# Performance work log

Hardware: AMD Instinct MI355X
Metric: run time of the kernel (lower is better)

The kernel has to match this reference:

```python
import math
import jax, jax.numpy as jnp
import numpy as np

NHEAD = 8


def setup_inputs() -> dict:
    key = jax.random.key(0)
    ks = jax.random.split(key, 16)
    B, S, M, Ss, Ksn, D = 8, 512, 8, 16, 16, 512
    f32 = jnp.float32
    w_scale = 0.05
    return {
        "q_temporal": jax.random.normal(ks[0], (B, S, M, D), f32),
        "k_temporal": jax.random.normal(ks[1], (B, S, M, D), f32),
        "v_temporal": jax.random.normal(ks[2], (B, S, M, D), f32),
        "q_static": jax.random.normal(ks[3], (B, Ss, D), f32),
        "k_static": jax.random.normal(ks[4], (B, Ksn, D), f32),
        "v_static": jax.random.normal(ks[5], (B, Ksn, D), f32),
        "mask_temporal": jax.random.randint(ks[6], (B, S, M), 0, 2).astype(jnp.int32),
        "mask_static": jax.random.randint(ks[7], (B, Ksn), 0, 2).astype(jnp.int32),
        "Wq": jax.random.normal(ks[8], (D, D), f32) * w_scale,
        "bq": jax.random.normal(ks[9], (D,), f32) * w_scale,
        "Wk": jax.random.normal(ks[10], (D, D), f32) * w_scale,
        "bk": jax.random.normal(ks[11], (D,), f32) * w_scale,
        "Wv": jax.random.normal(ks[12], (D, D), f32) * w_scale,
        "bv": jax.random.normal(ks[13], (D,), f32) * w_scale,
        "Wo": jax.random.normal(ks[14], (D, D), f32) * w_scale,
        "bo": jax.random.normal(ks[15], (D,), f32) * w_scale,
    }


def reference(q_temporal, k_temporal, v_temporal, q_static, k_static, v_static,
              mask_temporal, mask_static, Wq, bq, Wk, bk, Wv, bv, Wo, bo):
    B, S, M, D = q_temporal.shape
    dh = D // NHEAD
    scale = 1.0 / math.sqrt(dh)
    SM = S * M

    def lin(x, W, b):
        return x @ W + b

    def h5(x):  # [B,S,M,D] -> [B,H,S,M,dh]
        b, s, m, d = x.shape
        return x.reshape(b, s, m, NHEAD, dh).transpose(0, 3, 1, 2, 4)

    def h4(x):  # [B,N,D] -> [B,H,N,dh]
        b, n, d = x.shape
        return x.reshape(b, n, NHEAD, dh).transpose(0, 2, 1, 3)

    # additive masks: 1 -> 0 (keep), 0 -> -inf
    m_t = jnp.where(mask_temporal == 1, 0.0, -jnp.inf)  # [B,S,M]
    m_s = jnp.where(mask_static == 1, 0.0, -jnp.inf)    # [B,Ks]

    # shared static-key/value heads: [B,H,Ks,dh]
    Ks_h = h4(lin(k_static, Wk, bk))
    Vs_h = h4(lin(v_static, Wv, bv))

    # ---- temporal side ----
    Qt = h5(lin(q_temporal, Wq, bq))   # [B,H,S,M,dh]
    Kt = h5(lin(k_temporal, Wk, bk))
    Vt = h5(lin(v_temporal, Wv, bv))
    qt_kt = jnp.einsum('bhsmd,bhsnd->bhsmn', Qt, Kt) * scale + m_t[:, None, :, None, :]   # [B,H,S,M,M]
    qt_ks = jnp.einsum('bhsmd,bhkd->bhsmk', Qt, Ks_h) * scale + m_s[:, None, None, None, :]  # [B,H,S,M,Ks]
    w_t = jax.nn.softmax(jnp.concatenate([qt_kt, qt_ks], axis=-1), axis=-1)  # [B,H,S,M,M+Ks]
    qkv_t = (jnp.einsum('bhsmn,bhsnd->bhsmd', w_t[..., :M], Vt)
             + jnp.einsum('bhsmk,bhkd->bhsmd', w_t[..., M:], Vs_h))          # [B,H,S,M,dh]
    out_t = lin(qkv_t.transpose(0, 2, 3, 1, 4).reshape(B, S, M, D), Wo, bo)  # [B,S,M,D]

    # ---- static side ----
    Qs = h4(lin(q_static, Wq, bq))                              # [B,H,Ss,dh]
    Kt_f = h4(lin(k_temporal.reshape(B, SM, D), Wk, bk))        # [B,H,S*M,dh]
    Vt_f = h4(lin(v_temporal.reshape(B, SM, D), Wv, bv))
    qs_kt = jnp.einsum('bhqd,bhnd->bhqn', Qs, Kt_f) * scale + m_t.reshape(B, 1, 1, SM)  # [B,H,Ss,S*M]
    qs_ks = jnp.einsum('bhqd,bhkd->bhqk', Qs, Ks_h) * scale + m_s[:, None, None, :]     # [B,H,Ss,Ks]
    w_s = jax.nn.softmax(jnp.concatenate([qs_kt, qs_ks], axis=-1), axis=-1)  # [B,H,Ss,S*M+Ks]
    qkv_s = (jnp.einsum('bhqn,bhnd->bhqd', w_s[..., :SM], Vt_f)
             + jnp.einsum('bhqk,bhkd->bhqd', w_s[..., SM:], Vs_h))           # [B,H,Ss,dh]
    Ss = qkv_s.shape[2]
    out_s = lin(qkv_s.transpose(0, 2, 1, 3).reshape(B, Ss, D), Wo, bo)       # [B,Ss,D]

    return (out_t, w_t, out_s, w_s)
```

## Files before the change

### kernel.cpp

```cpp
#include <hip/hip_runtime.h>
#include <hip/hip_bf16.h>

typedef __attribute__((ext_vector_type(8))) __bf16 bf16x8;
typedef __attribute__((ext_vector_type(4))) float f32x4;

__device__ __forceinline__ float b2f(unsigned short u) {
    unsigned int x = ((unsigned int)u) << 16;
    float f;
    __builtin_memcpy(&f, &x, 4);
    return f;
}
__device__ __forceinline__ unsigned short f2b(float f) {
    __hip_bfloat16 h = __float2bfloat16(f);
    unsigned short u;
    __builtin_memcpy(&u, &h, 2);
    return u;
}
union U4 { uint4 v; unsigned short u[8]; };

__global__ __launch_bounds__(256) void transpose512cvt4(
    const float* __restrict__ i0, const float* __restrict__ i1,
    const float* __restrict__ i2, const float* __restrict__ i3,
    unsigned short* __restrict__ o0, unsigned short* __restrict__ o1,
    unsigned short* __restrict__ o2, unsigned short* __restrict__ o3)
{
    const float* in = i0;
    unsigned short* out = o0;
    if (blockIdx.z == 1) { in = i1; out = o1; }
    else if (blockIdx.z == 2) { in = i2; out = o2; }
    else if (blockIdx.z == 3) { in = i3; out = o3; }
    __shared__ float tile[32][33];
    int tx = threadIdx.x & 31, ty = threadIdx.x >> 5;
    int bx = blockIdx.x, by = blockIdx.y;
    #pragma unroll
    for (int i = 0; i < 32; i += 8)
        tile[ty + i][tx] = in[(size_t)(bx * 32 + ty + i) * 512 + by * 32 + tx];
    __syncthreads();
    #pragma unroll
    for (int i = 0; i < 32; i += 8)
        out[(size_t)(by * 32 + ty + i) * 512 + bx * 32 + tx] = f2b(tile[tx][ty + i]);
}


struct GemmSet {
    const void* A;
    const unsigned short* B;
    const float* bias;
    void* C;
    int cmode;
};

template<bool AF32>
__global__ __launch_bounds__(512, 2) void gemm_bp(
    GemmSet s0, GemmSet s1, GemmSet s2, int M, int mgroups)
{
    const int K = 512, N = 512;
    __shared__ __align__(16) unsigned short Bs[128 * 256];

    int NB = gridDim.x, bid = blockIdx.x;
    int wid;
    if ((NB & 31) == 0) {
        int x = bid & 7, tt = bid >> 3, r = tt & 3, j = tt >> 2;
        wid = (j * 8 + x) * 4 + r;
    } else wid = bid;
    int q = wid >> 2, np = wid & 3;
    int g = q / mgroups, mg = q - g * mgroups;
    GemmSet S = (g == 0) ? s0 : ((g == 1) ? s1 : s2);
    int n0 = np * 128, m0 = mg * 512;

    int t = threadIdx.x;
    int w = t >> 6, lane = t & 63, quad = lane >> 4, l16 = lane & 15;
    bool active = (m0 + w * 64) < M;
    size_t mrow = (size_t)(m0 + w * 64 + l16);

    const float* Ap32 = (const float*)S.A + mrow * K + quad * 8;
    const unsigned short* Ap16 = (const unsigned short*)S.A + mrow * K + quad * 8;

    int srow = t >> 2, sseg = t & 3;
    const unsigned short* Bg = S.B + (size_t)(n0 + srow) * K + sseg * 64;
    char* Bsb = (char*)Bs;
    unsigned int wbase = ((unsigned int)srow << 9) + ((unsigned int)sseg << 7);
    unsigned int wxor = ((unsigned int)(srow & 7)) << 4;
    unsigned int rxor = ((unsigned int)(l16 & 7)) << 4;

    f32x4 acc[4][8];
    #pragma unroll
    for (int i = 0; i < 4; ++i)
        #pragma unroll
        for (int j = 0; j < 8; ++j) acc[i][j] = (f32x4){0.f, 0.f, 0.f, 0.f};

    float4 pf[8];
    uint4 ph[4];

    auto ALOAD = [&](int kk) {
        if constexpr (AF32) {
            #pragma unroll
            for (int i = 0; i < 4; ++i) {
                const float4* pp = (const float4*)(Ap32 + (size_t)i * 16 * K + kk);
                pf[2 * i] = pp[0]; pf[2 * i + 1] = pp[1];
            }
        } else {
            #pragma unroll
            for (int i = 0; i < 4; ++i)
                ph[i] = *(const uint4*)(Ap16 + (size_t)i * 16 * K + kk);
        }
    };
    auto ACVT = [&](bf16x8* af) {
        if constexpr (AF32) {
            #pragma unroll
            for (int i = 0; i < 4; ++i) {
                U4 u;
                u.u[0] = f2b(pf[2*i].x);   u.u[1] = f2b(pf[2*i].y);
                u.u[2] = f2b(pf[2*i].z);   u.u[3] = f2b(pf[2*i].w);
                u.u[4] = f2b(pf[2*i+1].x); u.u[5] = f2b(pf[2*i+1].y);
                u.u[6] = f2b(pf[2*i+1].z); u.u[7] = f2b(pf[2*i+1].w);
                af[i] = *(bf16x8*)&u;
            }
        } else {
            #pragma unroll
            for (int i = 0; i < 4; ++i) af[i] = *(bf16x8*)&ph[i];
        }
    };
    auto STAGE = [&](int p) {
        uint4 v[8];
        #pragma unroll
        for (int i = 0; i < 8; ++i)
            v[i] = *(const uint4*)(Bg + p * 256 + i * 8);
        #pragma unroll
        for (int i = 0; i < 8; ++i)
            *(uint4*)(Bsb + ((wbase + i * 16) ^ wxor)) = v[i];
    };

    if (active) ALOAD(0);
    #pragma unroll
    for (int p = 0; p < 2; ++p) {
        __syncthreads();
        STAGE(p);
        __syncthreads();
        if (active) {
            int kb = p * 256;
            for (int ks = 0; ks < 8; ++ks) {
                bf16x8 af[4];
                ACVT(af);
                if (ks < 7) ALOAD(kb + (ks + 1) * 32);
                else if (p == 0) ALOAD(256);
                unsigned int kl2b = (unsigned int)((ks * 32 + quad * 8) * 2);
                #pragma unroll
                for (int j = 0; j < 8; ++j) {
                    unsigned int rb = (((unsigned int)(j * 16 + l16)) << 9) + kl2b;
                    bf16x8 bf = *(const bf16x8*)(Bsb + (rb ^ rxor));
                    #pragma unroll
                    for (int i = 0; i < 4; ++i)
                        acc[i][j] = __builtin_amdgcn_mfma_f32_16x16x32_bf16(af[i], bf, acc[i][j], 0, 0, 0);
                }
            }
        }
    }

    if (!active) return;
    int cmode = S.cmode;
    #pragma unroll
    for (int j = 0; j < 8; ++j) {
        int col = n0 + j * 16 + l16;
        float bc = S.bias[col];
        #pragma unroll
        for (int i = 0; i < 4; ++i) {
            int row = m0 + w * 64 + i * 16 + quad * 4;
            #pragma unroll
            for (int ii = 0; ii < 4; ++ii) {
                float v = acc[i][j][ii] + bc;
                int R = row + ii;
                if (cmode == 0) {
                    ((float*)S.C)[(size_t)R * N + col] = v;
                } else if (cmode == 1) {
                    ((unsigned short*)S.C)[(size_t)R * N + col] = f2b(v);
                } else {
                    int bb = R >> 12, n = R & 4095, hh = col >> 6, d = col & 63;
                    ((unsigned short*)S.C)[(((size_t)bb * 8 + hh) * 4096 + n) * 64 + d] = f2b(v);
                }
            }
        }
    }
}

__global__ __launch_bounds__(512) void temporal_attn(
    const unsigned short* __restrict__ Qt, const unsigned short* __restrict__ KH,
    const unsigned short* __restrict__ VH, const unsigned short* __restrict__ Ksp,
    const unsigned short* __restrict__ Vsp,
    const int* __restrict__ mask_t, const int* __restrict__ mask_s,
    float* __restrict__ w_t_out, unsigned short* __restrict__ qkv_t)
{
    int blk = blockIdx.x;
    int b = blk >> 8, sp = blk & 255;
    int s0 = sp * 2;
    int t = threadIdx.x;
    int h = t >> 6, lane = t & 63, quad = lane >> 4, l16 = lane & 15;

    __shared__ __align__(16) unsigned short Vt[8][64 * 40];
    __shared__ __align__(16) unsigned short Pl[8][16 * 40];

    size_t bh = (size_t)(b * 8 + h);
    size_t tok0 = ((size_t)(b * 512 + s0)) * 8;

    {
        int r = lane & 31, dh = (lane >> 5) * 32;
        const unsigned short* src = (r < 16)
            ? VH + (bh * 4096 + (size_t)(s0 * 8 + r)) * 64 + dh
            : Vsp + ((size_t)(b * 16 + (r - 16))) * 512 + h * 64 + dh;
        U4 u[4];
        #pragma unroll
        for (int g = 0; g < 4; ++g) u[g].v = ((const uint4*)src)[g];
        unsigned short* dst = &Vt[h][0];
        #pragma unroll
        for (int g = 0; g < 4; ++g)
            #pragma unroll
            for (int ii = 0; ii < 8; ++ii)
                dst[(dh + g * 8 + ii) * 40 + r] = u[g].u[ii];
    }

    const unsigned short* qp = Qt + (tok0 + l16) * 512 + h * 64 + quad * 8;
    bf16x8 qf0 = *(const bf16x8*)qp;
    bf16x8 qf1 = *(const bf16x8*)(qp + 32);
    const unsigned short* kpt = KH + (bh * 4096 + (size_t)(s0 * 8 + l16)) * 64 + quad * 8;
    bf16x8 kt0 = *(const bf16x8*)kpt;
    bf16x8 kt1 = *(const bf16x8*)(kpt + 32);
    const unsigned short* kps = Ksp + ((size_t)(b * 16 + l16)) * 512 + h * 64 + quad * 8;
    bf16x8 ks0 = *(const bf16x8*)kps;
    bf16x8 ks1 = *(const bf16x8*)(kps + 32);

    f32x4 sc0 = (f32x4){0.f, 0.f, 0.f, 0.f};
    f32x4 sc1 = (f32x4){0.f, 0.f, 0.f, 0.f};
    sc0 = __builtin_amdgcn_mfma_f32_16x16x32_bf16(qf0, kt0, sc0, 0, 0, 0);
    sc0 = __builtin_amdgcn_mfma_f32_16x16x32_bf16(qf1, kt1, sc0, 0, 0, 0);
    sc1 = __builtin_amdgcn_mfma_f32_16x16x32_bf16(qf0, ks0, sc1, 0, 0, 0);
    sc1 = __builtin_amdgcn_mfma_f32_16x16x32_bf16(qf1, ks1, sc1, 0, 0, 0);

    float madd0 = mask_t[tok0 + l16] ? 0.f : -1e30f;
    bool v0 = ((quad < 2) == (l16 < 8));
    if (!v0) madd0 = -1e30f;
    float madd1 = mask_s[b * 16 + l16] ? 0.f : -1e30f;

    float w0[4], w1[4];
    #pragma unroll
    for (int i = 0; i < 4; ++i) {
        float a = sc0[i] * 0.125f + madd0;
        float c = sc1[i] * 0.125f + madd1;
        float mx = fmaxf(a, c);
        mx = fmaxf(mx, __shfl_xor(mx, 1));
        mx = fmaxf(mx, __shfl_xor(mx, 2));
        mx = fmaxf(mx, __shfl_xor(mx, 4));
        mx = fmaxf(mx, __shfl_xor(mx, 8));
        float e0 = __expf(a - mx), e1 = __expf(c - mx);
        float se = e0 + e1;
        se += __shfl_xor(se, 1);
        se += __shfl_xor(se, 2);
        se += __shfl_xor(se, 4);
        se += __shfl_xor(se, 8);
        float inv = 1.f / se;
        w0[i] = e0 * inv;
        w1[i] = e1 * inv;
    }

    int row0 = quad * 4;
    #pragma unroll
    for (int i = 0; i < 4; ++i) {
        int row = row0 + i;
        Pl[h][row * 40 + l16] = f2b(w0[i]);
        Pl[h][row * 40 + 16 + l16] = f2b(w1[i]);
        int s = s0 + (row >> 3), m = row & 7;
        size_t wb = ((((size_t)b * 8 + h) * 512 + s) * 8 + m) * 24;
        if (v0) w_t_out[wb + (l16 & 7)] = w0[i];
        w_t_out[wb + 8 + l16] = w1[i];
    }

    bf16x8 pa = *(const bf16x8*)&Pl[h][l16 * 40 + quad * 8];
    f32x4 oacc[4];
    #pragma unroll
    for (int j = 0; j < 4; ++j) {
        bf16x8 vb = *(const bf16x8*)&Vt[h][(j * 16 + l16) * 40 + quad * 8];
        oacc[j] = (f32x4){0.f, 0.f, 0.f, 0.f};
        oacc[j] = __builtin_amdgcn_mfma_f32_16x16x32_bf16(pa, vb, oacc[j], 0, 0, 0);
    }
    #pragma unroll
    for (int j = 0; j < 4; ++j)
        #pragma unroll
        for (int ii = 0; ii < 4; ++ii) {
            int row = quad * 4 + ii;
            qkv_t[(tok0 + row) * 512 + h * 64 + j * 16 + l16] = f2b(oacc[j][ii]);
        }
}

__global__ __launch_bounds__(256) void static_attn_s1(
    const unsigned short* __restrict__ Qsp, const unsigned short* __restrict__ KH,
    const unsigned short* __restrict__ VH, const unsigned short* __restrict__ Ksp,
    const unsigned short* __restrict__ Vsp,
    const int* __restrict__ mask_t, const int* __restrict__ mask_s,
    float* __restrict__ w_s, float* __restrict__ Ppart, float* __restrict__ Lpart)
{
    int blk = blockIdx.x;
    int bh = blk & 63, c = blk >> 6;
    int b = bh >> 3, h = bh & 7;
    __shared__ __align__(16) unsigned short Klds[32 * 72];
    __shared__ __align__(16) unsigned short Vlds[64 * 40];
    __shared__ __align__(16) unsigned short Plds[16 * 40];
    __shared__ float maskv[32];
    __shared__ float sL[2][16];
    int t = threadIdx.x, wave = t >> 6, lane = t & 63, quad = lane >> 4, l16 = lane & 15;

    bf16x8 qf0 = *(const bf16x8*)(Qsp + ((size_t)(b * 16 + l16)) * 512 + h * 64 + quad * 8);
    bf16x8 qf1 = *(const bf16x8*)(Qsp + ((size_t)(b * 16 + l16)) * 512 + h * 64 + 32 + quad * 8);

    f32x4 pacc = (f32x4){0.f, 0.f, 0.f, 0.f};
    float Lacc[4] = {0.f, 0.f, 0.f, 0.f};
    int d0 = wave * 16;
    int sub = wave >> 1;
    int sr = t >> 3, spart = t & 7;
    int s0 = c * 16, s1 = (c == 7) ? 129 : (s0 + 16);

    for (int st = s0; st < s1; ++st) {
        int key0 = st * 32;
        int kk = key0 + sr;
        uint4 kv = {0, 0, 0, 0}, vv = {0, 0, 0, 0};
        if (kk < 4096) {
            kv = *(const uint4*)(KH + (((size_t)bh) * 4096 + kk) * 64 + spart * 8);
            vv = *(const uint4*)(VH + (((size_t)bh) * 4096 + kk) * 64 + spart * 8);
        } else if (kk < 4112) {
            kv = *(const uint4*)(Ksp + ((size_t)(b * 16 + kk - 4096)) * 512 + h * 64 + spart * 8);
            vv = *(const uint4*)(Vsp + ((size_t)(b * 16 + kk - 4096)) * 512 + h * 64 + spart * 8);
        }
        __syncthreads();
        *(uint4*)&Klds[sr * 72 + spart * 8] = kv;
        {
            U4 u; u.v = vv;
            #pragma unroll
            for (int ii = 0; ii < 8; ++ii) Vlds[(spart * 8 + ii) * 40 + sr] = u.u[ii];
        }
        if (t < 32) {
            int k2 = key0 + t;
            float ma = -1e30f;
            if (k2 < 4096) ma = mask_t[b * 4096 + k2] ? 0.f : -1e30f;
            else if (k2 < 4112) ma = mask_s[b * 16 + k2 - 4096] ? 0.f : -1e30f;
            maskv[t] = ma;
        }
        __syncthreads();
        if ((wave & 1) == 0) {
            bf16x8 kf0 = *(const bf16x8*)&Klds[(sub * 16 + l16) * 72 + quad * 8];
            bf16x8 kf1 = *(const bf16x8*)&Klds[(sub * 16 + l16) * 72 + 32 + quad * 8];
            f32x4 sc = (f32x4){0.f, 0.f, 0.f, 0.f};
            sc = __builtin_amdgcn_mfma_f32_16x16x32_bf16(qf0, kf0, sc, 0, 0, 0);
            sc = __builtin_amdgcn_mfma_f32_16x16x32_bf16(qf1, kf1, sc, 0, 0, 0);
            float ma = maskv[sub * 16 + l16];
            size_t wbase = (((size_t)bh) * 16 + quad * 4) * 4112 + key0 + sub * 16 + l16;
            #pragma unroll
            for (int i = 0; i < 4; ++i) {
                float sv = sc[i] * 0.125f + ma;
                float w = __expf(sv);
                Lacc[i] += w;
                w_s[wbase + (size_t)i * 4112] = w;
                Plds[(quad * 4 + i) * 40 + sub * 16 + l16] = f2b(w);
            }
        }
        __syncthreads();
        bf16x8 pf = *(const bf16x8*)&Plds[l16 * 40 + quad * 8];
        bf16x8 vf = *(const bf16x8*)&Vlds[(d0 + l16) * 40 + quad * 8];
        pacc = __builtin_amdgcn_mfma_f32_16x16x32_bf16(pf, vf, pacc, 0, 0, 0);
    }

    if ((wave & 1) == 0) {
        #pragma unroll
        for (int i = 0; i < 4; ++i) {
            float v = Lacc[i];
            v += __shfl_xor(v, 1);
            v += __shfl_xor(v, 2);
            v += __shfl_xor(v, 4);
            v += __shfl_xor(v, 8);
            Lacc[i] = v;
        }
        if (l16 == 0) {
            #pragma unroll
            for (int i = 0; i < 4; ++i) sL[wave >> 1][quad * 4 + i] = Lacc[i];
        }
    }
    size_t pbase = ((size_t)(bh * 8 + c) * 16 + quad * 4) * 64 + d0 + l16;
    #pragma unroll
    for (int i = 0; i < 4; ++i) Ppart[pbase + (size_t)i * 64] = pacc[i];
    __syncthreads();
    if (t < 16) Lpart[(bh * 8 + c) * 16 + t] = sL[0][t] + sL[1][t];
}

__global__ __launch_bounds__(256) void static_attn_s4(
    const float* __restrict__ Ppart, const float* __restrict__ Lpart,
    float* __restrict__ w_s, unsigned short* __restrict__ qkvS)
{
    int bh = blockIdx.x, b = bh >> 3, h = bh & 7;
    __shared__ float invL[16];
    int t = threadIdx.x;
    if (t < 16) {
        float L = 0.f;
        #pragma unroll
        for (int cc = 0; cc < 8; ++cc) L += Lpart[(bh * 8 + cc) * 16 + t];
        invL[t] = 1.f / L;
    }
    __syncthreads();
    #pragma unroll
    for (int i = 0; i < 4; ++i) {
        int idx = t + i * 256;
        int q = idx >> 6, d = idx & 63;
        float s = 0.f;
        #pragma unroll
        for (int cc = 0; cc < 8; ++cc) s += Ppart[((size_t)(bh * 8 + cc) * 16 + q) * 64 + d];
        qkvS[((size_t)(b * 16 + q)) * 512 + h * 64 + d] = f2b(s * invL[q]);
    }
    size_t base = (size_t)bh * 16 * 4112;
    for (int q = 0; q < 16; ++q) {
        float il = invL[q];
        for (int kk = t; kk < 4112; kk += 256) w_s[base + q * 4112 + kk] *= il;
    }
}

extern "C" void kernel_launch(void* const* d_in, const int* in_sizes, int n_in,
                              void* d_out, int out_size, void* d_ws, size_t ws_size,
                              hipStream_t stream)
{
    const float* q_t = (const float*)d_in[0];
    const float* k_t = (const float*)d_in[1];
    const float* v_t = (const float*)d_in[2];
    const float* q_s = (const float*)d_in[3];
    const float* k_s = (const float*)d_in[4];
    const float* v_s = (const float*)d_in[5];
    const int* m_t = (const int*)d_in[6];
    const int* m_s = (const int*)d_in[7];
    const float* Wq = (const float*)d_in[8];
    const float* bq = (const float*)d_in[9];
    const float* Wk = (const float*)d_in[10];
    const float* bk = (const float*)d_in[11];
    const float* Wv = (const float*)d_in[12];
    const float* bv = (const float*)d_in[13];
    const float* Wo = (const float*)d_in[14];
    const float* bo = (const float*)d_in[15];

    char* ws = (char*)d_ws;
    size_t off = 0;
    auto alloc = [&](size_t bytes) {
        void* p = ws + off;
        off += (bytes + 255) & ~(size_t)255;
        return p;
    };
    const size_t WB = (size_t)512 * 512 * 2;
    const size_t TB = (size_t)32768 * 512 * 2;
    const size_t SB = (size_t)128 * 512 * 2;
    unsigned short* WqT = (unsigned short*)alloc(WB);
    unsigned short* WkT = (unsigned short*)alloc(WB);
    unsigned short* WvT = (unsigned short*)alloc(WB);
    unsigned short* WoT = (unsigned short*)alloc(WB);
    unsigned short* Qt   = (unsigned short*)alloc(TB);
    unsigned short* KH   = (unsigned short*)alloc(TB);
    unsigned short* VH   = (unsigned short*)alloc(TB);
    unsigned short* qkvT = (unsigned short*)alloc(TB);
    unsigned short* Qsp  = (unsigned short*)alloc(SB);
    unsigned short* Ksp  = (unsigned short*)alloc(SB);
    unsigned short* Vsp  = (unsigned short*)alloc(SB);
    unsigned short* qkvS = (unsigned short*)alloc(SB);
    float* Ppart = (float*)alloc((size_t)64 * 8 * 16 * 64 * 4);
    float* Lpart = (float*)alloc((size_t)64 * 8 * 16 * 4);

    float* out    = (float*)d_out;
    float* out_tp = out;
    float* w_t_o  = out + 16777216;
    float* out_sp = out + 23068672;
    float* w_s_o  = out + 23134208;

    transpose512cvt4<<<dim3(16, 16, 4), 256, 0, stream>>>(Wq, Wk, Wv, Wo, WqT, WkT, WvT, WoT);

    GemmSet gq  = { q_t,  WqT, bq, Qt,   1 };
    GemmSet gk  = { k_t,  WkT, bk, KH,   2 };
    GemmSet gv  = { v_t,  WvT, bv, VH,   2 };
    GemmSet gqs = { q_s,  WqT, bq, Qsp,  1 };
    GemmSet gks = { k_s,  WkT, bk, Ksp,  1 };
    GemmSet gvs = { v_s,  WvT, bv, Vsp,  1 };
    GemmSet got = { qkvT, WoT, bo, out_tp, 0 };
    GemmSet gos = { qkvS, WoT, bo, out_sp, 0 };

    gemm_bp<true><<<dim3(768), 512, 0, stream>>>(gq, gk, gv, 32768, 64);
    gemm_bp<true><<<dim3(12), 512, 0, stream>>>(gqs, gks, gvs, 128, 1);

    temporal_attn<<<2048, 512, 0, stream>>>(Qt, KH, VH, Ksp, Vsp, m_t, m_s, w_t_o, qkvT);
    static_attn_s1<<<512, 256, 0, stream>>>(Qsp, KH, VH, Ksp, Vsp, m_t, m_s, w_s_o, Ppart, Lpart);
    static_attn_s4<<<64, 256, 0, stream>>>(Ppart, Lpart, w_s_o, qkvS);

    gemm_bp<false><<<dim3(256), 512, 0, stream>>>(got, got, got, 32768, 64);
    gemm_bp<false><<<dim3(4), 512, 0, stream>>>(gos, gos, gos, 128, 1);
}
```

Measured before the change: 582.7 us.

## Rewrite projection GEMMs with 128x128 tiles and async global-to-LDS double buffering

Replaces the 512-row by 128-column GEMM, which staged only B in LDS and kept A in registers, with a 128x128 tile kernel. Both A and B now stream through LDS in double-buffered 32-wide K slices using global_load_lds DMA with XOR swizzling. Block IDs are remapped so consecutive tiles land on the same XCD. The change is meant to cut register pressure, raise occupancy (256 threads, 3 blocks per CU), and overlap loads with MFMA work, at the cost of more blocks, more re-reads of A and B across tiles, and a barrier per K step.

```diff
diff --git a/kernel.cpp b/kernel.cpp
--- a/kernel.cpp
+++ b/kernel.cpp
@@ -17,6 +17,12 @@
     return u;
 }
 union U4 { uint4 v; unsigned short u[8]; };
+
+__device__ __forceinline__ void gload16(const void* g, void* l) {
+    __builtin_amdgcn_global_load_lds(
+        (const __attribute__((address_space(1))) unsigned int*)g,
+        (__attribute__((address_space(3))) unsigned int*)l, 16, 0, 0);
+}
 
 __global__ __launch_bounds__(256) void transpose512cvt4(
     const float* __restrict__ i0, const float* __restrict__ i1,
@@ -51,121 +57,116 @@
 };
 
 template<bool AF32>
-__global__ __launch_bounds__(512, 2) void gemm_bp(
-    GemmSet s0, GemmSet s1, GemmSet s2, int M, int mgroups)
+__global__ __launch_bounds__(256, 3) void gemm_lds(
+    GemmSet s0, GemmSet s1, GemmSet s2, int M)
 {
     const int K = 512, N = 512;
-    __shared__ __align__(16) unsigned short Bs[128 * 256];
+    __shared__ __align__(16) unsigned char AsB[AF32 ? 32768 : 16384];
+    __shared__ __align__(16) unsigned char BsB[16384];
 
     int NB = gridDim.x, bid = blockIdx.x;
-    int wid;
-    if ((NB & 31) == 0) {
-        int x = bid & 7, tt = bid >> 3, r = tt & 3, j = tt >> 2;
-        wid = (j * 8 + x) * 4 + r;
-    } else wid = bid;
-    int q = wid >> 2, np = wid & 3;
-    int g = q / mgroups, mg = q - g * mgroups;
+    int qq = NB >> 3, rr = NB & 7, xcd = bid & 7, idx = bid >> 3;
+    int wid = (xcd < rr ? xcd * (qq + 1) : rr * (qq + 1) + (xcd - rr) * qq) + idx;
+
+    int mtiles = M >> 7;
+    int np = wid & 3, t2 = wid >> 2;
+    int mt = t2 % mtiles, g = t2 / mtiles;
     GemmSet S = (g == 0) ? s0 : ((g == 1) ? s1 : s2);
-    int n0 = np * 128, m0 = mg * 512;
+    int m0 = mt * 128, n0 = np * 128;
 
     int t = threadIdx.x;
     int w = t >> 6, lane = t & 63, quad = lane >> 4, l16 = lane & 15;
-    bool active = (m0 + w * 64) < M;
-    size_t mrow = (size_t)(m0 + w * 64 + l16);
-
-    const float* Ap32 = (const float*)S.A + mrow * K + quad * 8;
-    const unsigned short* Ap16 = (const unsigned short*)S.A + mrow * K + quad * 8;
-
-    int srow = t >> 2, sseg = t & 3;
-    const unsigned short* Bg = S.B + (size_t)(n0 + srow) * K + sseg * 64;
-    char* Bsb = (char*)Bs;
-    unsigned int wbase = ((unsigned int)srow << 9) + ((unsigned int)sseg << 7);
-    unsigned int wxor = ((unsigned int)(srow & 7)) << 4;
-    unsigned int rxor = ((unsigned int)(l16 & 7)) << 4;
-
-    f32x4 acc[4][8];
+    int wr = w >> 1, wc = w & 1;
+
+    const float* Ap32 = (const float*)S.A;
+    const unsigned short* Ap16 = (const unsigned short*)S.A;
+    const unsigned short* Bp = S.B;
+
+    f32x4 acc[4][4];
     #pragma unroll
     for (int i = 0; i < 4; ++i)
         #pragma unroll
-        for (int j = 0; j < 8; ++j) acc[i][j] = (f32x4){0.f, 0.f, 0.f, 0.f};
-
-    float4 pf[8];
-    uint4 ph[4];
-
-    auto ALOAD = [&](int kk) {
+        for (int j = 0; j < 4; ++j) acc[i][j] = (f32x4){0.f, 0.f, 0.f, 0.f};
+
+    auto STAGE = [&](int buf, int k0) {
         if constexpr (AF32) {
             #pragma unroll
-            for (int i = 0; i < 4; ++i) {
-                const float4* pp = (const float4*)(Ap32 + (size_t)i * 16 * K + kk);
-                pf[2 * i] = pp[0]; pf[2 * i + 1] = pp[1];
+            for (int s = 0; s < 4; ++s) {
+                int r0 = w * 32 + s * 8;
+                int row = r0 + (lane >> 3);
+                int g2 = (lane & 7) ^ (row & 7);
+                gload16(Ap32 + (size_t)(m0 + row) * K + k0 + g2 * 4,
+                        AsB + buf * 16384 + r0 * 128);
             }
         } else {
             #pragma unroll
-            for (int i = 0; i < 4; ++i)
-                ph[i] = *(const uint4*)(Ap16 + (size_t)i * 16 * K + kk);
+            for (int s = 0; s < 2; ++s) {
+                int r0 = w * 32 + s * 16;
+                int row = r0 + (lane >> 2);
+                int g2 = (lane & 3) ^ ((row >> 1) & 3);
+                gload16(Ap16 + (size_t)(m0 + row) * K + k0 + g2 * 8,
+                        AsB + buf * 8192 + r0 * 64);
+            }
+        }
+        #pragma unroll
+        for (int s = 0; s < 2; ++s) {
+            int r0 = w * 32 + s * 16;
+            int row = r0 + (lane >> 2);
+            int g2 = (lane & 3) ^ ((row >> 1) & 3);
+            gload16(Bp + (size_t)(n0 + row) * K + k0 + g2 * 8,
+                    BsB + buf * 8192 + r0 * 64);
         }
     };
-    auto ACVT = [&](bf16x8* af) {
-        if constexpr (AF32) {
-            #pragma unroll
-            for (int i = 0; i < 4; ++i) {
+
+    auto COMPUTE = [&](int buf) {
+        bf16x8 af[4], bfj[4];
+        #pragma unroll
+        for (int j = 0; j < 4; ++j) {
+            int r = wc * 64 + j * 16 + l16;
+            bfj[j] = *(const bf16x8*)(BsB + buf * 8192 + r * 64
+                                      + ((quad ^ ((r >> 1) & 3)) * 16));
+        }
+        #pragma unroll
+        for (int i = 0; i < 4; ++i) {
+            int r = wr * 64 + i * 16 + l16;
+            if constexpr (AF32) {
+                const float4* rowp = (const float4*)(AsB + buf * 16384 + r * 128);
+                float4 f0 = rowp[(2 * quad) ^ (r & 7)];
+                float4 f1 = rowp[(2 * quad + 1) ^ (r & 7)];
                 U4 u;
-                u.u[0] = f2b(pf[2*i].x);   u.u[1] = f2b(pf[2*i].y);
-                u.u[2] = f2b(pf[2*i].z);   u.u[3] = f2b(pf[2*i].w);
-                u.u[4] = f2b(pf[2*i+1].x); u.u[5] = f2b(pf[2*i+1].y);
-                u.u[6] = f2b(pf[2*i+1].z); u.u[7] = f2b(pf[2*i+1].w);
+                u.u[0] = f2b(f0.x); u.u[1] = f2b(f0.y); u.u[2] = f2b(f0.z); u.u[3] = f2b(f0.w);
+                u.u[4] = f2b(f1.x); u.u[5] = f2b(f1.y); u.u[6] = f2b(f1.z); u.u[7] = f2b(f1.w);
                 af[i] = *(bf16x8*)&u;
+            } else {
+                af[i] = *(const bf16x8*)(AsB + buf * 8192 + r * 64
+                                         + ((quad ^ ((r >> 1) & 3)) * 16));
             }
-        } else {
-            #pragma unroll
-            for (int i = 0; i < 4; ++i) af[i] = *(bf16x8*)&ph[i];
-        }
+        }
+        #pragma unroll
+        for (int i = 0; i < 4; ++i)
+            #pragma unroll
+            for (int j = 0; j < 4; ++j)
+                acc[i][j] = __builtin_amdgcn_mfma_f32_16x16x32_bf16(af[i], bfj[j], acc[i][j], 0, 0, 0);
     };
-    auto STAGE = [&](int p) {
-        uint4 v[8];
-        #pragma unroll
-        for (int i = 0; i < 8; ++i)
-            v[i] = *(const uint4*)(Bg + p * 256 + i * 8);
-        #pragma unroll
-        for (int i = 0; i < 8; ++i)
-            *(uint4*)(Bsb + ((wbase + i * 16) ^ wxor)) = v[i];
-    };
-
-    if (active) ALOAD(0);
-    #pragma unroll
-    for (int p = 0; p < 2; ++p) {
+
+    STAGE(0, 0);
+    __syncthreads();
+    #pragma unroll 2
+    for (int it = 0; it < 16; ++it) {
+        int cur = it & 1;
+        if (it < 15) STAGE(cur ^ 1, (it + 1) * 32);
+        COMPUTE(cur);
         __syncthreads();
-        STAGE(p);
-        __syncthreads();
-        if (active) {
-            int kb = p * 256;
-            for (int ks = 0; ks < 8; ++ks) {
-                bf16x8 af[4];
-                ACVT(af);
-                if (ks < 7) ALOAD(kb + (ks + 1) * 32);
-                else if (p == 0) ALOAD(256);
-                unsigned int kl2b = (unsigned int)((ks * 32 + quad * 8) * 2);
-                #pragma unroll
-                for (int j = 0; j < 8; ++j) {
-                    unsigned int rb = (((unsigned int)(j * 16 + l16)) << 9) + kl2b;
-                    bf16x8 bf = *(const bf16x8*)(Bsb + (rb ^ rxor));
-                    #pragma unroll
-                    for (int i = 0; i < 4; ++i)
-                        acc[i][j] = __builtin_amdgcn_mfma_f32_16x16x32_bf16(af[i], bf, acc[i][j], 0, 0, 0);
-                }
-            }
-        }
-    }
-
-    if (!active) return;
+    }
+
     int cmode = S.cmode;
     #pragma unroll
-    for (int j = 0; j < 8; ++j) {
-        int col = n0 + j * 16 + l16;
-        float bc = S.bias[col];
-        #pragma unroll
-        for (int i = 0; i < 4; ++i) {
-            int row = m0 + w * 64 + i * 16 + quad * 4;
+    for (int i = 0; i < 4; ++i) {
+        #pragma unroll
+        for (int j = 0; j < 4; ++j) {
+            int row = m0 + wr * 64 + i * 16 + quad * 4;
+            int col = n0 + wc * 64 + j * 16 + l16;
+            float bc = S.bias[col];
             #pragma unroll
             for (int ii = 0; ii < 4; ++ii) {
                 float v = acc[i][j][ii] + bc;
@@ -481,13 +482,13 @@
     GemmSet got = { qkvT, WoT, bo, out_tp, 0 };
     GemmSet gos = { qkvS, WoT, bo, out_sp, 0 };
 
-    gemm_bp<true><<<dim3(768), 512, 0, stream>>>(gq, gk, gv, 32768, 64);
-    gemm_bp<true><<<dim3(12), 512, 0, stream>>>(gqs, gks, gvs, 128, 1);
+    gemm_lds<true><<<dim3(3072), 256, 0, stream>>>(gq, gk, gv, 32768);
+    gemm_lds<true><<<dim3(12), 256, 0, stream>>>(gqs, gks, gvs, 128);
 
     temporal_attn<<<2048, 512, 0, stream>>>(Qt, KH, VH, Ksp, Vsp, m_t, m_s, w_t_o, qkvT);
     static_attn_s1<<<512, 256, 0, stream>>>(Qsp, KH, VH, Ksp, Vsp, m_t, m_s, w_s_o, Ppart, Lpart);
     static_attn_s4<<<64, 256, 0, stream>>>(Ppart, Lpart, w_s_o, qkvS);
 
-    gemm_bp<false><<<dim3(256), 512, 0, stream>>>(got, got, got, 32768, 64);
-    gemm_bp<false><<<dim3(4), 512, 0, stream>>>(gos, gos, gos, 128, 1);
-}
+    gemm_lds<false><<<dim3(1024), 256, 0, stream>>>(got, got, got, 32768);
+    gemm_lds<false><<<dim3(4), 256, 0, stream>>>(gos, gos, gos, 128);
+}
```

After: 550.6 us. 1.06x faster.
